# Kernel optimization log

Hardware: AMD Instinct MI355X
Metric: run time of the kernel (lower is better)

Reference implementation:

```python
import jax, jax.numpy as jnp
import numpy as np

B = 64         # number of hypernetwork samples (scenes)
N = 16384      # number of query points
SIZE_IN = 256
SIZE_H = 128
SIZE_OUT = 128


def setup_inputs() -> dict:
    key = jax.random.key(0)
    k0, k1, k2, k3, k4, k5, k6 = jax.random.split(key, 7)
    # scale weights like small init to keep activations sane
    kls0 = jax.random.normal(k0, (B, SIZE_H, SIZE_IN), dtype=jnp.float32) * 0.05
    kls1 = jax.random.normal(k1, (B, SIZE_OUT, SIZE_H), dtype=jnp.float32) * 0.05
    kls2 = jax.random.normal(k2, (B, SIZE_OUT, SIZE_IN), dtype=jnp.float32) * 0.05
    bias0 = jax.random.normal(k3, (B, SIZE_H), dtype=jnp.float32) * 0.05
    bias1 = jax.random.normal(k4, (B, SIZE_OUT), dtype=jnp.float32) * 0.05
    x = jax.random.normal(k5, (N, SIZE_IN), dtype=jnp.float32)
    batch_index = jax.random.randint(k6, (N,), 0, B, dtype=jnp.int64)
    return {
        "kls0": kls0, "kls1": kls1, "kls2": kls2,
        "bias0": bias0, "bias1": bias1,
        "x": x, "batch_index": batch_index,
    }


def reference(kls0, kls1, kls2, bias0, bias1, x, batch_index):
    bi = batch_index
    # net = F.linear(relu(x), kls0[bi], bias0[bi])  -> per-row GEMV with gathered weights
    net = jnp.einsum("nhi,ni->nh", kls0[bi], jax.nn.relu(x)) + bias0[bi]
    # dx = F.linear(relu(net), kls1[bi], bias1[bi])
    dx = jnp.einsum("noh,nh->no", kls1[bi], jax.nn.relu(net)) + bias1[bi]
    # shortcut (size_in != size_out): x_s = F.linear(x, kls2[bi])
    x_s = jnp.einsum("noi,ni->no", kls2[bi], x)
    return x_s + dx
```

## Files before the change

### kernel.cpp

```cpp
#include <hip/hip_runtime.h>

#define NSCENE 64
#define NPTS   16384
#define SIN    256
#define SH     128
#define SOUT   128
#define TILE_P 32

#define WS_PARTIAL 0
#define WS_OFFSETS 16384
#define WS_PERM    17408
#define WS_WBF16   82944
#define W0_ELEMS   (NSCENE*SH*SIN)
#define W1_ELEMS   (NSCENE*SOUT*SH)
#define W2_ELEMS   (NSCENE*SOUT*SIN)
#define WTOT       (W0_ELEMS+W1_ELEMS+W2_ELEMS)
#define CONV_BLOCKS 2560

typedef __attribute__((ext_vector_type(8))) short bf16x8;
typedef __attribute__((ext_vector_type(4))) float f32x4;

__device__ __forceinline__ short f2bf(float f) {
  unsigned int u = __float_as_uint(f);
  unsigned int r = (u + 0x7FFFu + ((u >> 16) & 1u)) >> 16;
  return (short)(r & 0xFFFFu);
}


__global__ __launch_bounds__(256) void prep_kernel(
    const int* __restrict__ bidx,
    const float* __restrict__ kls0, const float* __restrict__ kls1,
    const float* __restrict__ kls2,
    int* __restrict__ partial, short* __restrict__ wb)
{
  int b = blockIdx.x;
  int tid = threadIdx.x;
  if (b < 64) {
    __shared__ int lh[NSCENE];
    if (tid < NSCENE) lh[tid] = 0;
    __syncthreads();
    atomicAdd(&lh[bidx[b * 256 + tid]], 1);
    __syncthreads();
    if (tid < NSCENE) partial[b * 64 + tid] = lh[tid];
  } else {
    int g = (b - 64) * 256 + tid;
    int e = g * 8;
    if (e < WTOT) {
      const float* src;
      if (e < W0_ELEMS) src = kls0 + e;
      else if (e < W0_ELEMS + W1_ELEMS) src = kls1 + (e - W0_ELEMS);
      else src = kls2 + (e - W0_ELEMS - W1_ELEMS);
      float4 u0 = *reinterpret_cast<const float4*>(src);
      float4 u1 = *reinterpret_cast<const float4*>(src + 4);
      bf16x8 v = (bf16x8){f2bf(u0.x), f2bf(u0.y), f2bf(u0.z), f2bf(u0.w),
                          f2bf(u1.x), f2bf(u1.y), f2bf(u1.z), f2bf(u1.w)};
      *reinterpret_cast<bf16x8*>(wb + e) = v;
    }
  }
}


__global__ __launch_bounds__(256) void scatter_kernel(
    const int* __restrict__ bidx, const int* __restrict__ partial,
    int* __restrict__ offsets, int* __restrict__ perm)
{
  __shared__ int cur[NSCENE];
  int b = blockIdx.x;
  int tid = threadIdx.x;
  if (tid < 64) {
    int s = tid;
    int colpre = 0, total = 0;
    for (int bb = 0; bb < 64; ++bb) {
      int v = partial[bb * 64 + s];
      if (bb < b) colpre += v;
      total += v;
    }
    int v = total;
    for (int off = 1; off < 64; off <<= 1) {
      int t = __shfl_up(v, off);
      if (s >= off) v += t;
    }
    int sceneoff = v - total;
    cur[s] = sceneoff + colpre;
    if (b == 0) {
      offsets[s] = sceneoff;
      if (s == 63) offsets[64] = NPTS;
    }
  }
  __syncthreads();
  int n = b * 256 + tid;
  int s = bidx[n];
  int pos = atomicAdd(&cur[s], 1);
  perm[pos] = n;
}


template<bool BF16W>
__global__ __launch_bounds__(256) void fused_kernel(
    const float* __restrict__ kls0, const float* __restrict__ kls1,
    const float* __restrict__ kls2, const float* __restrict__ bias0,
    const float* __restrict__ bias1, const float* __restrict__ x,
    const int* __restrict__ offsets, const int* __restrict__ perm,
    const short* __restrict__ wb, float* __restrict__ out)
{
  __shared__ __align__(16) short xr[TILE_P][SIN + 8];
  __shared__ __align__(16) short xp[TILE_P][SIN + 8];
  __shared__ __align__(16) short snet[TILE_P][SH + 8];
  __shared__ int ptile[TILE_P];

  const int s    = blockIdx.x & 63;
  const int t0   = blockIdx.x >> 6;
  const int base = offsets[s];
  const int cnt  = offsets[s + 1] - base;
  const int tid  = threadIdx.x;
  const int lane = tid & 63;
  const int w    = tid >> 6;
  const int l15  = lane & 15;
  const int lh4  = lane >> 4;

  const float* W0 = kls0 + (size_t)s * SH * SIN;
  const float* W1 = kls1 + (size_t)s * SOUT * SH;
  const float* W2 = kls2 + (size_t)s * SOUT * SIN;
  const short* B0 = wb + (size_t)s * SH * SIN;
  const short* B1 = wb + W0_ELEMS + (size_t)s * SOUT * SH;
  const short* B2 = wb + W0_ELEMS + W1_ELEMS + (size_t)s * SOUT * SIN;

  for (int t = t0; t * TILE_P < cnt; t += 8) {
    __syncthreads();

    {
      int r  = tid >> 3;
      int cg = tid & 7;
      int prow = t * TILE_P + r;
      int np = (prow < cnt) ? perm[base + prow] : -1;
      if (cg == 0) ptile[r] = np;
      const float* xrow = x + (size_t)(np < 0 ? 0 : np) * SIN;
      int c0 = cg * 32;
      for (int j = 0; j < 32; j += 4) {
        float4 v = make_float4(0.f, 0.f, 0.f, 0.f);
        if (np >= 0) v = *reinterpret_cast<const float4*>(xrow + c0 + j);
        short4 p, q;
        p.x = f2bf(v.x); p.y = f2bf(v.y); p.z = f2bf(v.z); p.w = f2bf(v.w);
        q.x = f2bf(fmaxf(v.x, 0.f)); q.y = f2bf(fmaxf(v.y, 0.f));
        q.z = f2bf(fmaxf(v.z, 0.f)); q.w = f2bf(fmaxf(v.w, 0.f));
        *reinterpret_cast<short4*>(&xp[r][c0 + j]) = p;
        *reinterpret_cast<short4*>(&xr[r][c0 + j]) = q;
      }
    }
    __syncthreads();

    f32x4 acc0[2][2];
    for (int nt2 = 0; nt2 < 2; ++nt2) {
      float bv = bias0[(size_t)s * SH + w * 32 + nt2 * 16 + l15];
      for (int mt = 0; mt < 2; ++mt) acc0[mt][nt2] = (f32x4){bv, bv, bv, bv};
    }
    for (int ks = 0; ks < 8; ++ks) {
      int kc = ks * 32 + lh4 * 8;
      bf16x8 bfrag[2];
      for (int nt2 = 0; nt2 < 2; ++nt2) {
        int row = w * 32 + nt2 * 16 + l15;
        if constexpr (BF16W) {
          bfrag[nt2] = *reinterpret_cast<const bf16x8*>(B0 + (size_t)row * SIN + kc);
        } else {
          const float* wr = W0 + (size_t)row * SIN + kc;
          float4 u0 = *reinterpret_cast<const float4*>(wr);
          float4 u1 = *reinterpret_cast<const float4*>(wr + 4);
          bfrag[nt2] = (bf16x8){f2bf(u0.x), f2bf(u0.y), f2bf(u0.z), f2bf(u0.w),
                                f2bf(u1.x), f2bf(u1.y), f2bf(u1.z), f2bf(u1.w)};
        }
      }
      for (int mt = 0; mt < 2; ++mt) {
        bf16x8 afrag = *reinterpret_cast<const bf16x8*>(&xr[mt * 16 + l15][kc]);
        for (int nt2 = 0; nt2 < 2; ++nt2)
          acc0[mt][nt2] = __builtin_amdgcn_mfma_f32_16x16x32_bf16(
              afrag, bfrag[nt2], acc0[mt][nt2], 0, 0, 0);
      }
    }
    for (int mt = 0; mt < 2; ++mt)
      for (int nt2 = 0; nt2 < 2; ++nt2)
        for (int r4 = 0; r4 < 4; ++r4)
          snet[mt * 16 + lh4 * 4 + r4][w * 32 + nt2 * 16 + l15] =
              f2bf(fmaxf(acc0[mt][nt2][r4], 0.f));

    f32x4 acc[2][2];
    for (int nt2 = 0; nt2 < 2; ++nt2) {
      float bv = bias1[(size_t)s * SOUT + w * 32 + nt2 * 16 + l15];
      for (int mt = 0; mt < 2; ++mt) acc[mt][nt2] = (f32x4){bv, bv, bv, bv};
    }
    for (int ks = 0; ks < 8; ++ks) {
      int kc = ks * 32 + lh4 * 8;
      bf16x8 bfrag[2];
      for (int nt2 = 0; nt2 < 2; ++nt2) {
        int row = w * 32 + nt2 * 16 + l15;
        if constexpr (BF16W) {
          bfrag[nt2] = *reinterpret_cast<const bf16x8*>(B2 + (size_t)row * SIN + kc);
        } else {
          const float* wr = W2 + (size_t)row * SIN + kc;
          float4 u0 = *reinterpret_cast<const float4*>(wr);
          float4 u1 = *reinterpret_cast<const float4*>(wr + 4);
          bfrag[nt2] = (bf16x8){f2bf(u0.x), f2bf(u0.y), f2bf(u0.z), f2bf(u0.w),
                                f2bf(u1.x), f2bf(u1.y), f2bf(u1.z), f2bf(u1.w)};
        }
      }
      for (int mt = 0; mt < 2; ++mt) {
        bf16x8 afrag = *reinterpret_cast<const bf16x8*>(&xp[mt * 16 + l15][kc]);
        for (int nt2 = 0; nt2 < 2; ++nt2)
          acc[mt][nt2] = __builtin_amdgcn_mfma_f32_16x16x32_bf16(
              afrag, bfrag[nt2], acc[mt][nt2], 0, 0, 0);
      }
    }
    __syncthreads();

    for (int ks = 0; ks < 4; ++ks) {
      int kc = ks * 32 + lh4 * 8;
      bf16x8 bfrag[2];
      for (int nt2 = 0; nt2 < 2; ++nt2) {
        int row = w * 32 + nt2 * 16 + l15;
        if constexpr (BF16W) {
          bfrag[nt2] = *reinterpret_cast<const bf16x8*>(B1 + (size_t)row * SH + kc);
        } else {
          const float* wr = W1 + (size_t)row * SH + kc;
          float4 u0 = *reinterpret_cast<const float4*>(wr);
          float4 u1 = *reinterpret_cast<const float4*>(wr + 4);
          bfrag[nt2] = (bf16x8){f2bf(u0.x), f2bf(u0.y), f2bf(u0.z), f2bf(u0.w),
                                f2bf(u1.x), f2bf(u1.y), f2bf(u1.z), f2bf(u1.w)};
        }
      }
      for (int mt = 0; mt < 2; ++mt) {
        bf16x8 afrag = *reinterpret_cast<const bf16x8*>(&snet[mt * 16 + l15][kc]);
        for (int nt2 = 0; nt2 < 2; ++nt2)
          acc[mt][nt2] = __builtin_amdgcn_mfma_f32_16x16x32_bf16(
              afrag, bfrag[nt2], acc[mt][nt2], 0, 0, 0);
      }
    }

    for (int mt = 0; mt < 2; ++mt)
      for (int r4 = 0; r4 < 4; ++r4) {
        int row = mt * 16 + lh4 * 4 + r4;
        int pt = ptile[row];
        if (pt >= 0) {
          for (int nt2 = 0; nt2 < 2; ++nt2)
            out[(size_t)pt * SOUT + w * 32 + nt2 * 16 + l15] = acc[mt][nt2][r4];
        }
      }
  }
}


extern "C" void kernel_launch(void* const* d_in, const int* in_sizes, int n_in,
                              void* d_out, int out_size, void* d_ws, size_t ws_size,
                              hipStream_t stream) {
  const float* kls0  = (const float*)d_in[0];
  const float* kls1  = (const float*)d_in[1];
  const float* kls2  = (const float*)d_in[2];
  const float* bias0 = (const float*)d_in[3];
  const float* bias1 = (const float*)d_in[4];
  const float* x     = (const float*)d_in[5];
  const int*   bidx  = (const int*)d_in[6];
  float* out = (float*)d_out;

  int*   partial = (int*)((char*)d_ws + WS_PARTIAL);
  int*   offsets = (int*)((char*)d_ws + WS_OFFSETS);
  int*   perm    = (int*)((char*)d_ws + WS_PERM);
  short* wb      = (short*)((char*)d_ws + WS_WBF16);

  bool bf16w = ws_size >= (size_t)WS_WBF16 + sizeof(short) * (size_t)WTOT;

  prep_kernel<<<bf16w ? (64 + CONV_BLOCKS) : 64, 256, 0, stream>>>(
      bidx, kls0, kls1, kls2, partial, wb);
  scatter_kernel<<<64, 256, 0, stream>>>(bidx, partial, offsets, perm);
  if (bf16w)
    fused_kernel<true><<<512, 256, 0, stream>>>(kls0, kls1, kls2, bias0, bias1,
                                                x, offsets, perm, wb, out);
  else
    fused_kernel<false><<<512, 256, 0, stream>>>(kls0, kls1, kls2, bias0, bias1,
                                                 x, offsets, perm, wb, out);
}
```

Baseline: 35.03 us.

## Merge scatter into prep kernel and use 8-wave blocks in fused kernel

Each of the 64 histogram blocks of the prep kernel now scans all indices, builds the full and prefix histograms and computes the scene offsets and the permutation itself. This removes the separate scatter kernel launch and its partial-histogram buffer. The fused kernel moves to 512 threads with 8 waves, each owning a 16-column slice. The W0 and W2 MFMAs are interleaved in one k-loop, and the bias and weight pointers are hoisted out of the tile loop. The cost is redundant histogram work (every block reads all 16K indices) and higher register pressure per block.

```diff
diff --git a/kernel.cpp b/kernel.cpp
--- a/kernel.cpp
+++ b/kernel.cpp
@@ -7,15 +7,14 @@
 #define SOUT   128
 #define TILE_P 32
 
-#define WS_PARTIAL 0
-#define WS_OFFSETS 16384
-#define WS_PERM    17408
-#define WS_WBF16   82944
+#define WS_OFFSETS 0
+#define WS_PERM    1024
+#define WS_WBF16   66560
 #define W0_ELEMS   (NSCENE*SH*SIN)
 #define W1_ELEMS   (NSCENE*SOUT*SH)
 #define W2_ELEMS   (NSCENE*SOUT*SIN)
 #define WTOT       (W0_ELEMS+W1_ELEMS+W2_ELEMS)
-#define CONV_BLOCKS 2560
+#define CONV_BLOCKS (WTOT/2048)
 
 typedef __attribute__((ext_vector_type(8))) short bf16x8;
 typedef __attribute__((ext_vector_type(4))) float f32x4;
@@ -31,20 +30,44 @@
     const int* __restrict__ bidx,
     const float* __restrict__ kls0, const float* __restrict__ kls1,
     const float* __restrict__ kls2,
-    int* __restrict__ partial, short* __restrict__ wb)
+    short* __restrict__ wb, int* __restrict__ offsets, int* __restrict__ perm)
 {
   int b = blockIdx.x;
   int tid = threadIdx.x;
   if (b < 64) {
-    __shared__ int lh[NSCENE];
-    if (tid < NSCENE) lh[tid] = 0;
-    __syncthreads();
-    atomicAdd(&lh[bidx[b * 256 + tid]], 1);
-    __syncthreads();
-    if (tid < NSCENE) partial[b * 64 + tid] = lh[tid];
+    __shared__ int histT[NSCENE];
+    __shared__ int histP[NSCENE];
+    __shared__ int cur[NSCENE];
+    if (tid < NSCENE) { histT[tid] = 0; histP[tid] = 0; }
+    __syncthreads();
+    int lim = b * 256;
+    for (int i = tid; i < NPTS; i += 256) {
+      int s = bidx[i];
+      atomicAdd(&histT[s], 1);
+      if (i < lim) atomicAdd(&histP[s], 1);
+    }
+    __syncthreads();
+    if (tid < NSCENE) {
+      int c = histT[tid];
+      int v = c;
+      for (int off = 1; off < 64; off <<= 1) {
+        int t = __shfl_up(v, off);
+        if (tid >= off) v += t;
+      }
+      int excl = v - c;
+      cur[tid] = excl + histP[tid];
+      if (b == 0) {
+        offsets[tid] = excl;
+        if (tid == 63) offsets[64] = NPTS;
+      }
+    }
+    __syncthreads();
+    int n = lim + tid;
+    int s = bidx[n];
+    int pos = atomicAdd(&cur[s], 1);
+    perm[pos] = n;
   } else {
-    int g = (b - 64) * 256 + tid;
-    int e = g * 8;
+    int e = ((b - 64) * 256 + tid) * 8;
     if (e < WTOT) {
       const float* src;
       if (e < W0_ELEMS) src = kls0 + e;
@@ -60,43 +83,8 @@
 }
 
 
-__global__ __launch_bounds__(256) void scatter_kernel(
-    const int* __restrict__ bidx, const int* __restrict__ partial,
-    int* __restrict__ offsets, int* __restrict__ perm)
-{
-  __shared__ int cur[NSCENE];
-  int b = blockIdx.x;
-  int tid = threadIdx.x;
-  if (tid < 64) {
-    int s = tid;
-    int colpre = 0, total = 0;
-    for (int bb = 0; bb < 64; ++bb) {
-      int v = partial[bb * 64 + s];
-      if (bb < b) colpre += v;
-      total += v;
-    }
-    int v = total;
-    for (int off = 1; off < 64; off <<= 1) {
-      int t = __shfl_up(v, off);
-      if (s >= off) v += t;
-    }
-    int sceneoff = v - total;
-    cur[s] = sceneoff + colpre;
-    if (b == 0) {
-      offsets[s] = sceneoff;
-      if (s == 63) offsets[64] = NPTS;
-    }
-  }
-  __syncthreads();
-  int n = b * 256 + tid;
-  int s = bidx[n];
-  int pos = atomicAdd(&cur[s], 1);
-  perm[pos] = n;
-}
-
-
 template<bool BF16W>
-__global__ __launch_bounds__(256) void fused_kernel(
+__global__ __launch_bounds__(512) void fused_kernel(
     const float* __restrict__ kls0, const float* __restrict__ kls1,
     const float* __restrict__ kls2, const float* __restrict__ bias0,
     const float* __restrict__ bias1, const float* __restrict__ x,
@@ -117,26 +105,30 @@
   const int w    = tid >> 6;
   const int l15  = lane & 15;
   const int lh4  = lane >> 4;
+  const int col  = w * 16 + l15;
 
   const float* W0 = kls0 + (size_t)s * SH * SIN;
   const float* W1 = kls1 + (size_t)s * SOUT * SH;
   const float* W2 = kls2 + (size_t)s * SOUT * SIN;
-  const short* B0 = wb + (size_t)s * SH * SIN;
-  const short* B1 = wb + W0_ELEMS + (size_t)s * SOUT * SH;
-  const short* B2 = wb + W0_ELEMS + W1_ELEMS + (size_t)s * SOUT * SIN;
+  const short* B0 = wb + (size_t)s * SH * SIN + (size_t)col * SIN;
+  const short* B1 = wb + W0_ELEMS + (size_t)s * SOUT * SH + (size_t)col * SH;
+  const short* B2 = wb + W0_ELEMS + W1_ELEMS + (size_t)s * SOUT * SIN + (size_t)col * SIN;
+
+  const float bv0 = bias0[(size_t)s * SH + col];
+  const float bv1 = bias1[(size_t)s * SOUT + col];
 
   for (int t = t0; t * TILE_P < cnt; t += 8) {
     __syncthreads();
 
     {
-      int r  = tid >> 3;
-      int cg = tid & 7;
+      int r  = tid >> 4;
+      int cg = tid & 15;
       int prow = t * TILE_P + r;
       int np = (prow < cnt) ? perm[base + prow] : -1;
       if (cg == 0) ptile[r] = np;
       const float* xrow = x + (size_t)(np < 0 ? 0 : np) * SIN;
-      int c0 = cg * 32;
-      for (int j = 0; j < 32; j += 4) {
+      int c0 = cg * 16;
+      for (int j = 0; j < 16; j += 4) {
         float4 v = make_float4(0.f, 0.f, 0.f, 0.f);
         if (np >= 0) v = *reinterpret_cast<const float4*>(xrow + c0 + j);
         short4 p, q;
@@ -149,99 +141,73 @@
     }
     __syncthreads();
 
-    f32x4 acc0[2][2];
-    for (int nt2 = 0; nt2 < 2; ++nt2) {
-      float bv = bias0[(size_t)s * SH + w * 32 + nt2 * 16 + l15];
-      for (int mt = 0; mt < 2; ++mt) acc0[mt][nt2] = (f32x4){bv, bv, bv, bv};
-    }
+    f32x4 acc0[2], acc[2];
+    for (int mt = 0; mt < 2; ++mt) {
+      acc0[mt] = (f32x4){bv0, bv0, bv0, bv0};
+      acc[mt]  = (f32x4){bv1, bv1, bv1, bv1};
+    }
+#pragma unroll
     for (int ks = 0; ks < 8; ++ks) {
       int kc = ks * 32 + lh4 * 8;
-      bf16x8 bfrag[2];
-      for (int nt2 = 0; nt2 < 2; ++nt2) {
-        int row = w * 32 + nt2 * 16 + l15;
-        if constexpr (BF16W) {
-          bfrag[nt2] = *reinterpret_cast<const bf16x8*>(B0 + (size_t)row * SIN + kc);
-        } else {
-          const float* wr = W0 + (size_t)row * SIN + kc;
-          float4 u0 = *reinterpret_cast<const float4*>(wr);
-          float4 u1 = *reinterpret_cast<const float4*>(wr + 4);
-          bfrag[nt2] = (bf16x8){f2bf(u0.x), f2bf(u0.y), f2bf(u0.z), f2bf(u0.w),
-                                f2bf(u1.x), f2bf(u1.y), f2bf(u1.z), f2bf(u1.w)};
-        }
-      }
+      bf16x8 b0f, b2f;
+      if constexpr (BF16W) {
+        b0f = *reinterpret_cast<const bf16x8*>(B0 + kc);
+        b2f = *reinterpret_cast<const bf16x8*>(B2 + kc);
+      } else {
+        const float* w0r = W0 + (size_t)col * SIN + kc;
+        const float* w2r = W2 + (size_t)col * SIN + kc;
+        float4 u0 = *reinterpret_cast<const float4*>(w0r);
+        float4 u1 = *reinterpret_cast<const float4*>(w0r + 4);
+        float4 v0 = *reinterpret_cast<const float4*>(w2r);
+        float4 v1 = *reinterpret_cast<const float4*>(w2r + 4);
+        b0f = (bf16x8){f2bf(u0.x), f2bf(u0.y), f2bf(u0.z), f2bf(u0.w),
+                       f2bf(u1.x), f2bf(u1.y), f2bf(u1.z), f2bf(u1.w)};
+        b2f = (bf16x8){f2bf(v0.x), f2bf(v0.y), f2bf(v0.z), f2bf(v0.w),
+                       f2bf(v1.x), f2bf(v1.y), f2bf(v1.z), f2bf(v1.w)};
+      }
+#pragma unroll
       for (int mt = 0; mt < 2; ++mt) {
-        bf16x8 afrag = *reinterpret_cast<const bf16x8*>(&xr[mt * 16 + l15][kc]);
-        for (int nt2 = 0; nt2 < 2; ++nt2)
-          acc0[mt][nt2] = __builtin_amdgcn_mfma_f32_16x16x32_bf16(
-              afrag, bfrag[nt2], acc0[mt][nt2], 0, 0, 0);
-      }
-    }
+        bf16x8 aR = *reinterpret_cast<const bf16x8*>(&xr[mt * 16 + l15][kc]);
+        bf16x8 aP = *reinterpret_cast<const bf16x8*>(&xp[mt * 16 + l15][kc]);
+        acc0[mt] = __builtin_amdgcn_mfma_f32_16x16x32_bf16(aR, b0f, acc0[mt], 0, 0, 0);
+        acc[mt]  = __builtin_amdgcn_mfma_f32_16x16x32_bf16(aP, b2f, acc[mt],  0, 0, 0);
+      }
+    }
+
+#pragma unroll
     for (int mt = 0; mt < 2; ++mt)
-      for (int nt2 = 0; nt2 < 2; ++nt2)
-        for (int r4 = 0; r4 < 4; ++r4)
-          snet[mt * 16 + lh4 * 4 + r4][w * 32 + nt2 * 16 + l15] =
-              f2bf(fmaxf(acc0[mt][nt2][r4], 0.f));
-
-    f32x4 acc[2][2];
-    for (int nt2 = 0; nt2 < 2; ++nt2) {
-      float bv = bias1[(size_t)s * SOUT + w * 32 + nt2 * 16 + l15];
-      for (int mt = 0; mt < 2; ++mt) acc[mt][nt2] = (f32x4){bv, bv, bv, bv};
-    }
-    for (int ks = 0; ks < 8; ++ks) {
-      int kc = ks * 32 + lh4 * 8;
-      bf16x8 bfrag[2];
-      for (int nt2 = 0; nt2 < 2; ++nt2) {
-        int row = w * 32 + nt2 * 16 + l15;
-        if constexpr (BF16W) {
-          bfrag[nt2] = *reinterpret_cast<const bf16x8*>(B2 + (size_t)row * SIN + kc);
-        } else {
-          const float* wr = W2 + (size_t)row * SIN + kc;
-          float4 u0 = *reinterpret_cast<const float4*>(wr);
-          float4 u1 = *reinterpret_cast<const float4*>(wr + 4);
-          bfrag[nt2] = (bf16x8){f2bf(u0.x), f2bf(u0.y), f2bf(u0.z), f2bf(u0.w),
-                                f2bf(u1.x), f2bf(u1.y), f2bf(u1.z), f2bf(u1.w)};
-        }
-      }
-      for (int mt = 0; mt < 2; ++mt) {
-        bf16x8 afrag = *reinterpret_cast<const bf16x8*>(&xp[mt * 16 + l15][kc]);
-        for (int nt2 = 0; nt2 < 2; ++nt2)
-          acc[mt][nt2] = __builtin_amdgcn_mfma_f32_16x16x32_bf16(
-              afrag, bfrag[nt2], acc[mt][nt2], 0, 0, 0);
-      }
-    }
-    __syncthreads();
-
+#pragma unroll
+      for (int r4 = 0; r4 < 4; ++r4)
+        snet[mt * 16 + lh4 * 4 + r4][col] = f2bf(fmaxf(acc0[mt][r4], 0.f));
+    __syncthreads();
+
+#pragma unroll
     for (int ks = 0; ks < 4; ++ks) {
       int kc = ks * 32 + lh4 * 8;
-      bf16x8 bfrag[2];
-      for (int nt2 = 0; nt2 < 2; ++nt2) {
-        int row = w * 32 + nt2 * 16 + l15;
-        if constexpr (BF16W) {
-          bfrag[nt2] = *reinterpret_cast<const bf16x8*>(B1 + (size_t)row * SH + kc);
-        } else {
-          const float* wr = W1 + (size_t)row * SH + kc;
-          float4 u0 = *reinterpret_cast<const float4*>(wr);
-          float4 u1 = *reinterpret_cast<const float4*>(wr + 4);
-          bfrag[nt2] = (bf16x8){f2bf(u0.x), f2bf(u0.y), f2bf(u0.z), f2bf(u0.w),
-                                f2bf(u1.x), f2bf(u1.y), f2bf(u1.z), f2bf(u1.w)};
-        }
-      }
+      bf16x8 b1f;
+      if constexpr (BF16W) {
+        b1f = *reinterpret_cast<const bf16x8*>(B1 + kc);
+      } else {
+        const float* w1r = W1 + (size_t)col * SH + kc;
+        float4 u0 = *reinterpret_cast<const float4*>(w1r);
+        float4 u1 = *reinterpret_cast<const float4*>(w1r + 4);
+        b1f = (bf16x8){f2bf(u0.x), f2bf(u0.y), f2bf(u0.z), f2bf(u0.w),
+                       f2bf(u1.x), f2bf(u1.y), f2bf(u1.z), f2bf(u1.w)};
+      }
+#pragma unroll
       for (int mt = 0; mt < 2; ++mt) {
-        bf16x8 afrag = *reinterpret_cast<const bf16x8*>(&snet[mt * 16 + l15][kc]);
-        for (int nt2 = 0; nt2 < 2; ++nt2)
-          acc[mt][nt2] = __builtin_amdgcn_mfma_f32_16x16x32_bf16(
-              afrag, bfrag[nt2], acc[mt][nt2], 0, 0, 0);
-      }
-    }
-
+        bf16x8 aS = *reinterpret_cast<const bf16x8*>(&snet[mt * 16 + l15][kc]);
+        acc[mt] = __builtin_amdgcn_mfma_f32_16x16x32_bf16(aS, b1f, acc[mt], 0, 0, 0);
+      }
+    }
+
+#pragma unroll
     for (int mt = 0; mt < 2; ++mt)
+#pragma unroll
       for (int r4 = 0; r4 < 4; ++r4) {
         int row = mt * 16 + lh4 * 4 + r4;
         int pt = ptile[row];
-        if (pt >= 0) {
-          for (int nt2 = 0; nt2 < 2; ++nt2)
-            out[(size_t)pt * SOUT + w * 32 + nt2 * 16 + l15] = acc[mt][nt2][r4];
-        }
+        if (pt >= 0) out[(size_t)pt * SOUT + col] = acc[mt][r4];
       }
   }
 }
@@ -259,7 +225,6 @@
   const int*   bidx  = (const int*)d_in[6];
   float* out = (float*)d_out;
 
-  int*   partial = (int*)((char*)d_ws + WS_PARTIAL);
   int*   offsets = (int*)((char*)d_ws + WS_OFFSETS);
   int*   perm    = (int*)((char*)d_ws + WS_PERM);
   short* wb      = (short*)((char*)d_ws + WS_WBF16);
@@ -267,12 +232,11 @@
   bool bf16w = ws_size >= (size_t)WS_WBF16 + sizeof(short) * (size_t)WTOT;
 
   prep_kernel<<<bf16w ? (64 + CONV_BLOCKS) : 64, 256, 0, stream>>>(
-      bidx, kls0, kls1, kls2, partial, wb);
-  scatter_kernel<<<64, 256, 0, stream>>>(bidx, partial, offsets, perm);
+      bidx, kls0, kls1, kls2, wb, offsets, perm);
   if (bf16w)
-    fused_kernel<true><<<512, 256, 0, stream>>>(kls0, kls1, kls2, bias0, bias1,
+    fused_kernel<true><<<512, 512, 0, stream>>>(kls0, kls1, kls2, bias0, bias1,
                                                 x, offsets, perm, wb, out);
   else
-    fused_kernel<false><<<512, 256, 0, stream>>>(kls0, kls1, kls2, bias0, bias1,
+    fused_kernel<false><<<512, 512, 0, stream>>>(kls0, kls1, kls2, bias0, bias1,
                                                  x, offsets, perm, wb, out);
 }
```

Measured after the change: 45.08 us. 1.29x slower.

## Give each wave its own 16-point tile over all output columns, removing block syncs

Applied to the files above, without the earlier changes.

Restructures the fused kernel so each wave independently handles a 16-point tile across all 128 output columns, instead of four waves sharing a 32-point tile split by columns. X rows are loaded straight from global into MFMA A-fragments, which removes the shared x staging buffers and every block-level barrier. The layer-0 and shortcut GEMMs are interleaved in one k-loop. This trades fewer barriers and less LDS traffic for higher register pressure (16 accumulator vectors) and more per-wave weight-fragment loads from L2, since each wave now reads the whole weight matrix itself.

```diff
diff --git a/kernel.cpp b/kernel.cpp
--- a/kernel.cpp
+++ b/kernel.cpp
@@ -5,7 +5,6 @@
 #define SIN    256
 #define SH     128
 #define SOUT   128
-#define TILE_P 32
 
 #define WS_PARTIAL 0
 #define WS_OFFSETS 16384
@@ -15,7 +14,7 @@
 #define W1_ELEMS   (NSCENE*SOUT*SH)
 #define W2_ELEMS   (NSCENE*SOUT*SIN)
 #define WTOT       (W0_ELEMS+W1_ELEMS+W2_ELEMS)
-#define CONV_BLOCKS 2560
+#define CONV_BLOCKS (WTOT/2048)
 
 typedef __attribute__((ext_vector_type(8))) short bf16x8;
 typedef __attribute__((ext_vector_type(4))) float f32x4;
@@ -43,8 +42,7 @@
     __syncthreads();
     if (tid < NSCENE) partial[b * 64 + tid] = lh[tid];
   } else {
-    int g = (b - 64) * 256 + tid;
-    int e = g * 8;
+    int e = ((b - 64) * 256 + tid) * 8;
     if (e < WTOT) {
       const float* src;
       if (e < W0_ELEMS) src = kls0 + e;
@@ -96,6 +94,18 @@
 
 
 template<bool BF16W>
+__device__ __forceinline__ bf16x8 ldw(const short* bptr, const float* fptr) {
+  if constexpr (BF16W) {
+    return *reinterpret_cast<const bf16x8*>(bptr);
+  } else {
+    float4 u0 = *reinterpret_cast<const float4*>(fptr);
+    float4 u1 = *reinterpret_cast<const float4*>(fptr + 4);
+    return (bf16x8){f2bf(u0.x), f2bf(u0.y), f2bf(u0.z), f2bf(u0.w),
+                    f2bf(u1.x), f2bf(u1.y), f2bf(u1.z), f2bf(u1.w)};
+  }
+}
+
+template<bool BF16W>
 __global__ __launch_bounds__(256) void fused_kernel(
     const float* __restrict__ kls0, const float* __restrict__ kls1,
     const float* __restrict__ kls2, const float* __restrict__ bias0,
@@ -103,13 +113,10 @@
     const int* __restrict__ offsets, const int* __restrict__ perm,
     const short* __restrict__ wb, float* __restrict__ out)
 {
-  __shared__ __align__(16) short xr[TILE_P][SIN + 8];
-  __shared__ __align__(16) short xp[TILE_P][SIN + 8];
-  __shared__ __align__(16) short snet[TILE_P][SH + 8];
-  __shared__ int ptile[TILE_P];
+  __shared__ __align__(16) short snet[4][16][SH + 8];
 
   const int s    = blockIdx.x & 63;
-  const int t0   = blockIdx.x >> 6;
+  const int b8   = blockIdx.x >> 6;
   const int base = offsets[s];
   const int cnt  = offsets[s + 1] - base;
   const int tid  = threadIdx.x;
@@ -125,124 +132,75 @@
   const short* B1 = wb + W0_ELEMS + (size_t)s * SOUT * SH;
   const short* B2 = wb + W0_ELEMS + W1_ELEMS + (size_t)s * SOUT * SIN;
 
-  for (int t = t0; t * TILE_P < cnt; t += 8) {
-    __syncthreads();
-
-    {
-      int r  = tid >> 3;
-      int cg = tid & 7;
-      int prow = t * TILE_P + r;
-      int np = (prow < cnt) ? perm[base + prow] : -1;
-      if (cg == 0) ptile[r] = np;
-      const float* xrow = x + (size_t)(np < 0 ? 0 : np) * SIN;
-      int c0 = cg * 32;
-      for (int j = 0; j < 32; j += 4) {
-        float4 v = make_float4(0.f, 0.f, 0.f, 0.f);
-        if (np >= 0) v = *reinterpret_cast<const float4*>(xrow + c0 + j);
-        short4 p, q;
-        p.x = f2bf(v.x); p.y = f2bf(v.y); p.z = f2bf(v.z); p.w = f2bf(v.w);
-        q.x = f2bf(fmaxf(v.x, 0.f)); q.y = f2bf(fmaxf(v.y, 0.f));
-        q.z = f2bf(fmaxf(v.z, 0.f)); q.w = f2bf(fmaxf(v.w, 0.f));
-        *reinterpret_cast<short4*>(&xp[r][c0 + j]) = p;
-        *reinterpret_cast<short4*>(&xr[r][c0 + j]) = q;
+  float bv0[8], bv1[8];
+#pragma unroll
+  for (int nt = 0; nt < 8; ++nt) {
+    bv0[nt] = bias0[(size_t)s * SH + nt * 16 + l15];
+    bv1[nt] = bias1[(size_t)s * SOUT + nt * 16 + l15];
+  }
+
+  short (*sn)[SH + 8] = snet[w];
+
+  for (int t = b8 * 4 + w; t * 16 < cnt; t += 32) {
+    int pr = t * 16 + l15;
+    int np = (pr < cnt) ? perm[base + pr] : -1;
+    const float* px = x + (size_t)(np < 0 ? 0 : np) * SIN;
+
+    f32x4 acc0[8], acc2[8];
+#pragma unroll
+    for (int nt = 0; nt < 8; ++nt) {
+      acc0[nt] = (f32x4){bv0[nt], bv0[nt], bv0[nt], bv0[nt]};
+      acc2[nt] = (f32x4){bv1[nt], bv1[nt], bv1[nt], bv1[nt]};
+    }
+
+#pragma unroll
+    for (int ks = 0; ks < 8; ++ks) {
+      const int kc = ks * 32 + lh4 * 8;
+      float4 u0 = *reinterpret_cast<const float4*>(px + kc);
+      float4 u1 = *reinterpret_cast<const float4*>(px + kc + 4);
+      bf16x8 aP = (bf16x8){f2bf(u0.x), f2bf(u0.y), f2bf(u0.z), f2bf(u0.w),
+                           f2bf(u1.x), f2bf(u1.y), f2bf(u1.z), f2bf(u1.w)};
+      bf16x8 aR = (bf16x8){f2bf(fmaxf(u0.x, 0.f)), f2bf(fmaxf(u0.y, 0.f)),
+                           f2bf(fmaxf(u0.z, 0.f)), f2bf(fmaxf(u0.w, 0.f)),
+                           f2bf(fmaxf(u1.x, 0.f)), f2bf(fmaxf(u1.y, 0.f)),
+                           f2bf(fmaxf(u1.z, 0.f)), f2bf(fmaxf(u1.w, 0.f))};
+#pragma unroll
+      for (int nt = 0; nt < 8; ++nt) {
+        const size_t wro = (size_t)(nt * 16 + l15) * SIN + kc;
+        bf16x8 b0f = ldw<BF16W>(B0 + wro, W0 + wro);
+        bf16x8 b2f = ldw<BF16W>(B2 + wro, W2 + wro);
+        acc0[nt] = __builtin_amdgcn_mfma_f32_16x16x32_bf16(aR, b0f, acc0[nt], 0, 0, 0);
+        acc2[nt] = __builtin_amdgcn_mfma_f32_16x16x32_bf16(aP, b2f, acc2[nt], 0, 0, 0);
       }
     }
-    __syncthreads();
-
-    f32x4 acc0[2][2];
-    for (int nt2 = 0; nt2 < 2; ++nt2) {
-      float bv = bias0[(size_t)s * SH + w * 32 + nt2 * 16 + l15];
-      for (int mt = 0; mt < 2; ++mt) acc0[mt][nt2] = (f32x4){bv, bv, bv, bv};
-    }
-    for (int ks = 0; ks < 8; ++ks) {
-      int kc = ks * 32 + lh4 * 8;
-      bf16x8 bfrag[2];
-      for (int nt2 = 0; nt2 < 2; ++nt2) {
-        int row = w * 32 + nt2 * 16 + l15;
-        if constexpr (BF16W) {
-          bfrag[nt2] = *reinterpret_cast<const bf16x8*>(B0 + (size_t)row * SIN + kc);
-        } else {
-          const float* wr = W0 + (size_t)row * SIN + kc;
-          float4 u0 = *reinterpret_cast<const float4*>(wr);
-          float4 u1 = *reinterpret_cast<const float4*>(wr + 4);
-          bfrag[nt2] = (bf16x8){f2bf(u0.x), f2bf(u0.y), f2bf(u0.z), f2bf(u0.w),
-                                f2bf(u1.x), f2bf(u1.y), f2bf(u1.z), f2bf(u1.w)};
-        }
+
+#pragma unroll
+    for (int nt = 0; nt < 8; ++nt)
+#pragma unroll
+      for (int r4 = 0; r4 < 4; ++r4)
+        sn[lh4 * 4 + r4][nt * 16 + l15] = f2bf(fmaxf(acc0[nt][r4], 0.f));
+
+#pragma unroll
+    for (int ks = 0; ks < 4; ++ks) {
+      const int kc = ks * 32 + lh4 * 8;
+      bf16x8 aS = *reinterpret_cast<const bf16x8*>(&sn[l15][kc]);
+#pragma unroll
+      for (int nt = 0; nt < 8; ++nt) {
+        const size_t wro = (size_t)(nt * 16 + l15) * SH + kc;
+        bf16x8 b1f = ldw<BF16W>(B1 + wro, W1 + wro);
+        acc2[nt] = __builtin_amdgcn_mfma_f32_16x16x32_bf16(aS, b1f, acc2[nt], 0, 0, 0);
       }
-      for (int mt = 0; mt < 2; ++mt) {
-        bf16x8 afrag = *reinterpret_cast<const bf16x8*>(&xr[mt * 16 + l15][kc]);
-        for (int nt2 = 0; nt2 < 2; ++nt2)
-          acc0[mt][nt2] = __builtin_amdgcn_mfma_f32_16x16x32_bf16(
-              afrag, bfrag[nt2], acc0[mt][nt2], 0, 0, 0);
+    }
+
+#pragma unroll
+    for (int r4 = 0; r4 < 4; ++r4) {
+      int pt = __shfl(np, lh4 * 4 + r4);
+      if (pt >= 0) {
+#pragma unroll
+        for (int nt = 0; nt < 8; ++nt)
+          out[(size_t)pt * SOUT + nt * 16 + l15] = acc2[nt][r4];
       }
     }
-    for (int mt = 0; mt < 2; ++mt)
-      for (int nt2 = 0; nt2 < 2; ++nt2)
-        for (int r4 = 0; r4 < 4; ++r4)
-          snet[mt * 16 + lh4 * 4 + r4][w * 32 + nt2 * 16 + l15] =
-              f2bf(fmaxf(acc0[mt][nt2][r4], 0.f));
-
-    f32x4 acc[2][2];
-    for (int nt2 = 0; nt2 < 2; ++nt2) {
-      float bv = bias1[(size_t)s * SOUT + w * 32 + nt2 * 16 + l15];
-      for (int mt = 0; mt < 2; ++mt) acc[mt][nt2] = (f32x4){bv, bv, bv, bv};
-    }
-    for (int ks = 0; ks < 8; ++ks) {
-      int kc = ks * 32 + lh4 * 8;
-      bf16x8 bfrag[2];
-      for (int nt2 = 0; nt2 < 2; ++nt2) {
-        int row = w * 32 + nt2 * 16 + l15;
-        if constexpr (BF16W) {
-          bfrag[nt2] = *reinterpret_cast<const bf16x8*>(B2 + (size_t)row * SIN + kc);
-        } else {
-          const float* wr = W2 + (size_t)row * SIN + kc;
-          float4 u0 = *reinterpret_cast<const float4*>(wr);
-          float4 u1 = *reinterpret_cast<const float4*>(wr + 4);
-          bfrag[nt2] = (bf16x8){f2bf(u0.x), f2bf(u0.y), f2bf(u0.z), f2bf(u0.w),
-                                f2bf(u1.x), f2bf(u1.y), f2bf(u1.z), f2bf(u1.w)};
-        }
-      }
-      for (int mt = 0; mt < 2; ++mt) {
-        bf16x8 afrag = *reinterpret_cast<const bf16x8*>(&xp[mt * 16 + l15][kc]);
-        for (int nt2 = 0; nt2 < 2; ++nt2)
-          acc[mt][nt2] = __builtin_amdgcn_mfma_f32_16x16x32_bf16(
-              afrag, bfrag[nt2], acc[mt][nt2], 0, 0, 0);
-      }
-    }
-    __syncthreads();
-
-    for (int ks = 0; ks < 4; ++ks) {
-      int kc = ks * 32 + lh4 * 8;
-      bf16x8 bfrag[2];
-      for (int nt2 = 0; nt2 < 2; ++nt2) {
-        int row = w * 32 + nt2 * 16 + l15;
-        if constexpr (BF16W) {
-          bfrag[nt2] = *reinterpret_cast<const bf16x8*>(B1 + (size_t)row * SH + kc);
-        } else {
-          const float* wr = W1 + (size_t)row * SH + kc;
-          float4 u0 = *reinterpret_cast<const float4*>(wr);
-          float4 u1 = *reinterpret_cast<const float4*>(wr + 4);
-          bfrag[nt2] = (bf16x8){f2bf(u0.x), f2bf(u0.y), f2bf(u0.z), f2bf(u0.w),
-                                f2bf(u1.x), f2bf(u1.y), f2bf(u1.z), f2bf(u1.w)};
-        }
-      }
-      for (int mt = 0; mt < 2; ++mt) {
-        bf16x8 afrag = *reinterpret_cast<const bf16x8*>(&snet[mt * 16 + l15][kc]);
-        for (int nt2 = 0; nt2 < 2; ++nt2)
-          acc[mt][nt2] = __builtin_amdgcn_mfma_f32_16x16x32_bf16(
-              afrag, bfrag[nt2], acc[mt][nt2], 0, 0, 0);
-      }
-    }
-
-    for (int mt = 0; mt < 2; ++mt)
-      for (int r4 = 0; r4 < 4; ++r4) {
-        int row = mt * 16 + lh4 * 4 + r4;
-        int pt = ptile[row];
-        if (pt >= 0) {
-          for (int nt2 = 0; nt2 < 2; ++nt2)
-            out[(size_t)pt * SOUT + w * 32 + nt2 * 16 + l15] = acc[mt][nt2][r4];
-        }
-      }
   }
 }
 
```

Measured after the change: 110.3 us. +214.9%, slower.
